# Kernel optimization log

Hardware: AMD Instinct MI355X
Metric: run time of the kernel (lower is better)

Reference implementation:

```python
import jax, jax.numpy as jnp
import numpy as np

EPS = 1e-5  # torch LayerNorm default


def setup_inputs() -> dict:
    key = jax.random.key(0)
    ks = jax.random.split(key, 7)
    B, s, i, c, h = 1, 1024, 512, 8, 8
    scale = 0.1
    return {
        "m": jax.random.normal(ks[0], (B, s, i, c), dtype=jnp.float32),
        "ln_gamma": jnp.ones((c,), dtype=jnp.float32),
        "ln_beta": jnp.zeros((c,), dtype=jnp.float32),
        "Wq": jax.random.normal(ks[1], (c * h, c), dtype=jnp.float32) * scale,
        "Wk": jax.random.normal(ks[2], (c, c), dtype=jnp.float32) * scale,
        "Wv": jax.random.normal(ks[3], (c, c), dtype=jnp.float32) * scale,
        "Wg": jax.random.normal(ks[4], (c * h, c), dtype=jnp.float32) * scale,
        "Wo": jax.random.normal(ks[5], (c, c * h), dtype=jnp.float32) * scale,
        "bo": jnp.zeros((c,), dtype=jnp.float32),
    }


def reference(m, ln_gamma, ln_beta, Wq, Wk, Wv, Wg, Wo, bo):
    c = Wk.shape[0]
    h = Wq.shape[0] // c
    B, s, i, _ = m.shape

    # LayerNorm over the channel dim c
    mu = jnp.mean(m, axis=-1, keepdims=True)
    var = jnp.mean(jnp.square(m - mu), axis=-1, keepdims=True)
    x = (m - mu) * jax.lax.rsqrt(var + EPS) * ln_gamma + ln_beta  # (B,s,i,c)

    # projections (torch Linear: y = x @ W.T)
    q = (x @ Wq.T).reshape(B, s, i, h, c).mean(axis=1)            # (B,i,h,c) mean-pooled query
    k = x @ Wk.T                                                   # (B,s,i,c)
    v = x @ Wv.T                                                   # (B,s,i,c)
    gate = jax.nn.sigmoid(x @ Wg.T).reshape(B, s, i, h, c)        # (B,s,i,h,c)

    # attention logits over the column axis t (=s), softmax along t (dim=-3 of b t i h)
    a = jnp.einsum('bihc,btic->btih', q, k) * (c ** -0.5)          # (B,s,i,h)
    a = jax.nn.softmax(a, axis=1)

    o = gate * jnp.einsum('btih,btic->btihc', a, v)               # (B,s,i,h,c)
    o = o.reshape(B, s, i, h * c)
    return o @ Wo.T + bo                                           # (B,s,i,c)
```

## Files before the change

kernel.cpp:

```cpp
#include <hip/hip_runtime.h>

namespace {
constexpr int S = 1024, I = 512, C = 8, H = 8;
constexpr float LNEPS = 1e-5f;
constexpr float SCALE = 0.35355339059327373f;
}

__device__ __forceinline__ float dot8(const float x[8], float4 a, float4 b) {
    float r = x[0] * a.x;
    r += x[1] * a.y; r += x[2] * a.z; r += x[3] * a.w;
    r += x[4] * b.x; r += x[5] * b.y; r += x[6] * b.z; r += x[7] * b.w;
    return r;
}

__device__ __forceinline__ void ln8(float4 a, float4 b, const float gm[8],
                                    const float bt[8], float x[8]) {
    x[0] = a.x; x[1] = a.y; x[2] = a.z; x[3] = a.w;
    x[4] = b.x; x[5] = b.y; x[6] = b.z; x[7] = b.w;
    float mu = 0.f;
#pragma unroll
    for (int c = 0; c < 8; c++) mu += x[c];
    mu *= 0.125f;
    float var = 0.f;
#pragma unroll
    for (int c = 0; c < 8; c++) { float d = x[c] - mu; var += d * d; }
    var *= 0.125f;
    float inv = rsqrtf(var + LNEPS);
#pragma unroll
    for (int c = 0; c < 8; c++) x[c] = (x[c] - mu) * inv * gm[c] + bt[c];
}

__global__ __launch_bounds__(256) void k1_part(const float* __restrict__ m,
                                               const float* __restrict__ gamma,
                                               const float* __restrict__ beta,
                                               float* __restrict__ part1, int CH1) {
    int g = blockIdx.x * 256 + threadIdx.x;
    int i = g & (I - 1);
    int sc = g >> 9;
    int niter = S / CH1;
    float gm[8], bt[8];
#pragma unroll
    for (int c = 0; c < 8; c++) { gm[c] = gamma[c]; bt[c] = beta[c]; }
    float acc[8];
#pragma unroll
    for (int c = 0; c < 8; c++) acc[c] = 0.f;
    const float4* m4 = (const float4*)m;
    for (int j = 0; j < niter; j++) {
        int row = (sc * niter + j) * I + i;
        float x[8];
        ln8(m4[row * 2], m4[row * 2 + 1], gm, bt, x);
#pragma unroll
        for (int c = 0; c < 8; c++) acc[c] += x[c];
    }
    float4* p4 = (float4*)&part1[((size_t)sc * I + i) * 8];
    p4[0] = make_float4(acc[0], acc[1], acc[2], acc[3]);
    p4[1] = make_float4(acc[4], acc[5], acc[6], acc[7]);
}

__global__ __launch_bounds__(64) void k1b_qk(const float* __restrict__ part1,
                                             const float* __restrict__ Wq,
                                             const float* __restrict__ Wk,
                                             float* __restrict__ qk, int CH1) {
    int i = blockIdx.x, t = threadIdx.x;
    float xs[8];
#pragma unroll
    for (int c = 0; c < 8; c++) xs[c] = 0.f;
    const float4* p4 = (const float4*)part1;
    for (int p = t; p < CH1; p += 64) {
        float4 a = p4[((size_t)p * I + i) * 2], b = p4[((size_t)p * I + i) * 2 + 1];
        xs[0] += a.x; xs[1] += a.y; xs[2] += a.z; xs[3] += a.w;
        xs[4] += b.x; xs[5] += b.y; xs[6] += b.z; xs[7] += b.w;
    }
#pragma unroll
    for (int d = 1; d < 64; d <<= 1)
#pragma unroll
        for (int c = 0; c < 8; c++) xs[c] += __shfl_xor(xs[c], d, 64);
    int h = t >> 3, c2 = t & 7;
    float acc = 0.f;
#pragma unroll
    for (int c = 0; c < 8; c++) {
        float qc = 0.f;
#pragma unroll
        for (int c3 = 0; c3 < 8; c3++) qc += xs[c3] * Wq[(h * 8 + c) * 8 + c3];
        acc += qc * Wk[c * 8 + c2];
    }
    qk[i * 64 + t] = acc * (SCALE / 1024.0f);
}

__global__ __launch_bounds__(256) void k2_part(const float* __restrict__ m,
                                               const float* __restrict__ gamma,
                                               const float* __restrict__ beta,
                                               const float* __restrict__ qk,
                                               float* __restrict__ part2, int CH2) {
    int g = blockIdx.x * 256 + threadIdx.x;
    int i = g & (I - 1);
    int sc = g >> 9;
    int niter = S / CH2;
    float gm[8], bt[8];
#pragma unroll
    for (int c = 0; c < 8; c++) { gm[c] = gamma[c]; bt[c] = beta[c]; }
    const float4* qk4 = (const float4*)qk;
    float4 qv[16];
#pragma unroll
    for (int j = 0; j < 16; j++) qv[j] = qk4[i * 16 + j];
    float acc[8];
#pragma unroll
    for (int h = 0; h < 8; h++) acc[h] = 0.f;
    const float4* m4 = (const float4*)m;
    for (int j0 = 0; j0 < niter; j0 += 4) {
        float x[4][8];
#pragma unroll
        for (int r = 0; r < 4; r++) {
            int row = (sc * niter + j0 + r) * I + i;
            ln8(m4[row * 2], m4[row * 2 + 1], gm, bt, x[r]);
        }
#pragma unroll
        for (int h = 0; h < 8; h++)
#pragma unroll
            for (int r = 0; r < 4; r++)
                acc[h] += __expf(dot8(x[r], qv[h * 2], qv[h * 2 + 1]));
    }
    float4* p4 = (float4*)&part2[((size_t)sc * I + i) * 8];
    p4[0] = make_float4(acc[0], acc[1], acc[2], acc[3]);
    p4[1] = make_float4(acc[4], acc[5], acc[6], acc[7]);
}

__global__ __launch_bounds__(64) void k2b_rden(const float* __restrict__ part2,
                                               float* __restrict__ rden, int CH2) {
    int i = blockIdx.x, t = threadIdx.x;
    float d[8];
#pragma unroll
    for (int c = 0; c < 8; c++) d[c] = 0.f;
    const float4* p4 = (const float4*)part2;
    for (int p = t; p < CH2; p += 64) {
        float4 a = p4[((size_t)p * I + i) * 2], b = p4[((size_t)p * I + i) * 2 + 1];
        d[0] += a.x; d[1] += a.y; d[2] += a.z; d[3] += a.w;
        d[4] += b.x; d[5] += b.y; d[6] += b.z; d[7] += b.w;
    }
#pragma unroll
    for (int dd = 1; dd < 64; dd <<= 1)
#pragma unroll
        for (int c = 0; c < 8; c++) d[c] += __shfl_xor(d[c], dd, 64);
    if (t < 8) rden[i * 8 + t] = 1.0f / d[t];
}

__global__ __launch_bounds__(256) void k3_out(const float* __restrict__ m,
                                              const float* __restrict__ gamma,
                                              const float* __restrict__ beta,
                                              const float* __restrict__ Wv,
                                              const float* __restrict__ Wg,
                                              const float* __restrict__ Wo,
                                              const float* __restrict__ bo,
                                              const float* __restrict__ qk,
                                              const float* __restrict__ rden,
                                              float* __restrict__ out) {
    __shared__ __align__(16) float sWv[64];
    __shared__ __align__(16) float sWg[512];
    __shared__ __align__(16) float sWoT[512];
    int t = threadIdx.x;
    if (t < 64) sWv[t] = Wv[t];
    sWg[t] = Wg[t];
    sWg[t + 256] = Wg[t + 256];
    {
        int j = t & 63, c2 = t >> 6;
        sWoT[j * 8 + c2] = Wo[c2 * 64 + j];
        sWoT[j * 8 + c2 + 4] = Wo[(c2 + 4) * 64 + j];
    }
    __syncthreads();

    float gm[8], bt[8], bov[8];
#pragma unroll
    for (int c = 0; c < 8; c++) { gm[c] = gamma[c]; bt[c] = beta[c]; bov[c] = bo[c]; }

    int g = blockIdx.x * 256 + t;
    int i = g & (I - 1);
    int sg = g >> 9;
    const float4* m4 = (const float4*)m;
    float4* out4 = (float4*)out;

    float4 xa[4], xb[4];
#pragma unroll
    for (int r = 0; r < 4; r++) {
        int row = (sg + 256 * r) * I + i;
        xa[r] = m4[row * 2]; xb[r] = m4[row * 2 + 1];
    }
    float x[4][8];
#pragma unroll
    for (int r = 0; r < 4; r++) ln8(xa[r], xb[r], gm, bt, x[r]);

    const float4* sWv4 = (const float4*)sWv;
    const float4* sWg4 = (const float4*)sWg;
    const float4* sWoT4 = (const float4*)sWoT;

    float v[4][8];
#pragma unroll
    for (int c = 0; c < 8; c++) {
        float4 w0 = sWv4[c * 2], w1 = sWv4[c * 2 + 1];
#pragma unroll
        for (int r = 0; r < 4; r++) v[r][c] = dot8(x[r], w0, w1);
    }

    float oacc[4][8];
#pragma unroll
    for (int r = 0; r < 4; r++)
#pragma unroll
        for (int c2 = 0; c2 < 8; c2++) oacc[r][c2] = bov[c2];

    const float4* qk4 = (const float4*)qk;
#pragma unroll 1
    for (int h = 0; h < 8; h++) {
        float4 q0 = qk4[i * 16 + h * 2], q1 = qk4[i * 16 + h * 2 + 1];
        float rd = rden[i * 8 + h];
        float a_[4];
#pragma unroll
        for (int r = 0; r < 4; r++) a_[r] = __expf(dot8(x[r], q0, q1)) * rd;
#pragma unroll
        for (int c = 0; c < 8; c++) {
            int hc = h * 8 + c;
            float4 wg0 = sWg4[hc * 2], wg1 = sWg4[hc * 2 + 1];
            float o_[4];
#pragma unroll
            for (int r = 0; r < 4; r++) {
                float z = dot8(x[r], wg0, wg1);
                float gate = __builtin_amdgcn_rcpf(1.0f + __expf(-z));
                o_[r] = gate * a_[r] * v[r][c];
            }
            float4 wo0 = sWoT4[hc * 2], wo1 = sWoT4[hc * 2 + 1];
#pragma unroll
            for (int r = 0; r < 4; r++) {
                oacc[r][0] += o_[r] * wo0.x; oacc[r][1] += o_[r] * wo0.y;
                oacc[r][2] += o_[r] * wo0.z; oacc[r][3] += o_[r] * wo0.w;
                oacc[r][4] += o_[r] * wo1.x; oacc[r][5] += o_[r] * wo1.y;
                oacc[r][6] += o_[r] * wo1.z; oacc[r][7] += o_[r] * wo1.w;
            }
        }
    }
#pragma unroll
    for (int r = 0; r < 4; r++) {
        int row = (sg + 256 * r) * I + i;
        out4[row * 2] = make_float4(oacc[r][0], oacc[r][1], oacc[r][2], oacc[r][3]);
        out4[row * 2 + 1] = make_float4(oacc[r][4], oacc[r][5], oacc[r][6], oacc[r][7]);
    }
}

extern "C" void kernel_launch(void* const* d_in, const int* in_sizes, int n_in,
                              void* d_out, int out_size, void* d_ws, size_t ws_size,
                              hipStream_t stream) {
    const float* m     = (const float*)d_in[0];
    const float* gamma = (const float*)d_in[1];
    const float* beta  = (const float*)d_in[2];
    const float* Wq    = (const float*)d_in[3];
    const float* Wk    = (const float*)d_in[4];
    const float* Wv    = (const float*)d_in[5];
    const float* Wg    = (const float*)d_in[6];
    const float* Wo    = (const float*)d_in[7];
    const float* bo    = (const float*)d_in[8];
    float* out = (float*)d_out;

    const size_t small = (size_t)I * 64 * 4 + (size_t)I * 8 * 4;
    int CH1 = 256, CH2 = 256;
    auto need = [&](int c1, int c2) {
        return ((size_t)(c1 + c2) * I * C * 4) + small;
    };
    if (need(256, 256) > ws_size) { CH1 = CH2 = 64; }
    if (need(CH1, CH2) > ws_size) { CH1 = CH2 = 16; }

    float* ws    = (float*)d_ws;
    float* part1 = ws;
    float* part2 = part1 + (size_t)CH1 * I * C;
    float* qk    = part2 + (size_t)CH2 * I * C;
    float* rden  = qk + (size_t)I * 64;

    k1_part<<<I * CH1 / 256, 256, 0, stream>>>(m, gamma, beta, part1, CH1);
    k1b_qk<<<I, 64, 0, stream>>>(part1, Wq, Wk, qk, CH1);
    k2_part<<<I * CH2 / 256, 256, 0, stream>>>(m, gamma, beta, qk, part2, CH2);
    k2b_rden<<<I, 64, 0, stream>>>(part2, rden, CH2);
    k3_out<<<I * 256 / 256, 256, 0, stream>>>(m, gamma, beta, Wv, Wg, Wo, bo, qk,
                                              rden, out);
}
```

Before: 131.7 us.

## Increase parallel split across s, widen reductions, and halve rows per thread in output kernel

The s-axis is now split into 512 chunks instead of 256, so the partial-sum and softmax-denominator kernels each process 2 rows per thread. The reduction kernels use 256 threads with a shared-memory cross-wave combine, and one workspace buffer is shared between both stages. The output kernel runs twice as many blocks, each thread handling 2 rows instead of 4, with launch bounds requesting higher occupancy. The aim is more parallelism and latency hiding, at the cost of more launches' worth of partial traffic and dropping the workspace-size fallback.

```diff
diff --git a/kernel.cpp b/kernel.cpp
--- a/kernel.cpp
+++ b/kernel.cpp
@@ -2,6 +2,7 @@
 
 namespace {
 constexpr int S = 1024, I = 512, C = 8, H = 8;
+constexpr int CH1 = 512, CH2 = 512;
 constexpr float LNEPS = 1e-5f;
 constexpr float SCALE = 0.35355339059327373f;
 }
@@ -33,11 +34,10 @@
 __global__ __launch_bounds__(256) void k1_part(const float* __restrict__ m,
                                                const float* __restrict__ gamma,
                                                const float* __restrict__ beta,
-                                               float* __restrict__ part1, int CH1) {
+                                               float* __restrict__ part1) {
     int g = blockIdx.x * 256 + threadIdx.x;
     int i = g & (I - 1);
     int sc = g >> 9;
-    int niter = S / CH1;
     float gm[8], bt[8];
 #pragma unroll
     for (int c = 0; c < 8; c++) { gm[c] = gamma[c]; bt[c] = beta[c]; }
@@ -45,8 +45,9 @@
 #pragma unroll
     for (int c = 0; c < 8; c++) acc[c] = 0.f;
     const float4* m4 = (const float4*)m;
-    for (int j = 0; j < niter; j++) {
-        int row = (sc * niter + j) * I + i;
+#pragma unroll
+    for (int j = 0; j < S / CH1; j++) {
+        int row = (sc * (S / CH1) + j) * I + i;
         float x[8];
         ln8(m4[row * 2], m4[row * 2 + 1], gm, bt, x);
 #pragma unroll
@@ -57,16 +58,19 @@
     p4[1] = make_float4(acc[4], acc[5], acc[6], acc[7]);
 }
 
-__global__ __launch_bounds__(64) void k1b_qk(const float* __restrict__ part1,
-                                             const float* __restrict__ Wq,
-                                             const float* __restrict__ Wk,
-                                             float* __restrict__ qk, int CH1) {
+__global__ __launch_bounds__(256) void k1b_qk(const float* __restrict__ part1,
+                                              const float* __restrict__ Wq,
+                                              const float* __restrict__ Wk,
+                                              float* __restrict__ qk) {
+    __shared__ float sred[4][8];
     int i = blockIdx.x, t = threadIdx.x;
     float xs[8];
 #pragma unroll
     for (int c = 0; c < 8; c++) xs[c] = 0.f;
     const float4* p4 = (const float4*)part1;
-    for (int p = t; p < CH1; p += 64) {
+#pragma unroll
+    for (int k = 0; k < CH1 / 256; k++) {
+        int p = t + 256 * k;
         float4 a = p4[((size_t)p * I + i) * 2], b = p4[((size_t)p * I + i) * 2 + 1];
         xs[0] += a.x; xs[1] += a.y; xs[2] += a.z; xs[3] += a.w;
         xs[4] += b.x; xs[5] += b.y; xs[6] += b.z; xs[7] += b.w;
@@ -75,64 +79,69 @@
     for (int d = 1; d < 64; d <<= 1)
 #pragma unroll
         for (int c = 0; c < 8; c++) xs[c] += __shfl_xor(xs[c], d, 64);
-    int h = t >> 3, c2 = t & 7;
-    float acc = 0.f;
-#pragma unroll
-    for (int c = 0; c < 8; c++) {
-        float qc = 0.f;
-#pragma unroll
-        for (int c3 = 0; c3 < 8; c3++) qc += xs[c3] * Wq[(h * 8 + c) * 8 + c3];
-        acc += qc * Wk[c * 8 + c2];
-    }
-    qk[i * 64 + t] = acc * (SCALE / 1024.0f);
-}
-
-__global__ __launch_bounds__(256) void k2_part(const float* __restrict__ m,
-                                               const float* __restrict__ gamma,
-                                               const float* __restrict__ beta,
-                                               const float* __restrict__ qk,
-                                               float* __restrict__ part2, int CH2) {
+    if ((t & 63) == 0) {
+#pragma unroll
+        for (int c = 0; c < 8; c++) sred[t >> 6][c] = xs[c];
+    }
+    __syncthreads();
+    if (t < 64) {
+#pragma unroll
+        for (int c = 0; c < 8; c++)
+            xs[c] = sred[0][c] + sred[1][c] + sred[2][c] + sred[3][c];
+        int h = t >> 3, c2 = t & 7;
+        float acc = 0.f;
+#pragma unroll
+        for (int c = 0; c < 8; c++) {
+            float qc = 0.f;
+#pragma unroll
+            for (int c3 = 0; c3 < 8; c3++) qc += xs[c3] * Wq[(h * 8 + c) * 8 + c3];
+            acc += qc * Wk[c * 8 + c2];
+        }
+        qk[i * 64 + t] = acc * (SCALE / 1024.0f);
+    }
+}
+
+__global__ __launch_bounds__(256, 4) void k2_part(const float* __restrict__ m,
+                                                  const float* __restrict__ gamma,
+                                                  const float* __restrict__ beta,
+                                                  const float* __restrict__ qk,
+                                                  float* __restrict__ part2) {
     int g = blockIdx.x * 256 + threadIdx.x;
     int i = g & (I - 1);
     int sc = g >> 9;
-    int niter = S / CH2;
     float gm[8], bt[8];
 #pragma unroll
     for (int c = 0; c < 8; c++) { gm[c] = gamma[c]; bt[c] = beta[c]; }
+    const float4* m4 = (const float4*)m;
+    float x[2][8];
+#pragma unroll
+    for (int r = 0; r < 2; r++) {
+        int row = (sc * 2 + r) * I + i;
+        ln8(m4[row * 2], m4[row * 2 + 1], gm, bt, x[r]);
+    }
     const float4* qk4 = (const float4*)qk;
-    float4 qv[16];
-#pragma unroll
-    for (int j = 0; j < 16; j++) qv[j] = qk4[i * 16 + j];
     float acc[8];
 #pragma unroll
-    for (int h = 0; h < 8; h++) acc[h] = 0.f;
-    const float4* m4 = (const float4*)m;
-    for (int j0 = 0; j0 < niter; j0 += 4) {
-        float x[4][8];
-#pragma unroll
-        for (int r = 0; r < 4; r++) {
-            int row = (sc * niter + j0 + r) * I + i;
-            ln8(m4[row * 2], m4[row * 2 + 1], gm, bt, x[r]);
-        }
-#pragma unroll
-        for (int h = 0; h < 8; h++)
-#pragma unroll
-            for (int r = 0; r < 4; r++)
-                acc[h] += __expf(dot8(x[r], qv[h * 2], qv[h * 2 + 1]));
+    for (int h = 0; h < 8; h++) {
+        float4 q0 = qk4[i * 16 + h * 2], q1 = qk4[i * 16 + h * 2 + 1];
+        acc[h] = __expf(dot8(x[0], q0, q1)) + __expf(dot8(x[1], q0, q1));
     }
     float4* p4 = (float4*)&part2[((size_t)sc * I + i) * 8];
     p4[0] = make_float4(acc[0], acc[1], acc[2], acc[3]);
     p4[1] = make_float4(acc[4], acc[5], acc[6], acc[7]);
 }
 
-__global__ __launch_bounds__(64) void k2b_rden(const float* __restrict__ part2,
-                                               float* __restrict__ rden, int CH2) {
+__global__ __launch_bounds__(256) void k2b_rden(const float* __restrict__ part2,
+                                                float* __restrict__ rden) {
+    __shared__ float sred[4][8];
     int i = blockIdx.x, t = threadIdx.x;
     float d[8];
 #pragma unroll
     for (int c = 0; c < 8; c++) d[c] = 0.f;
     const float4* p4 = (const float4*)part2;
-    for (int p = t; p < CH2; p += 64) {
+#pragma unroll
+    for (int k = 0; k < CH2 / 256; k++) {
+        int p = t + 256 * k;
         float4 a = p4[((size_t)p * I + i) * 2], b = p4[((size_t)p * I + i) * 2 + 1];
         d[0] += a.x; d[1] += a.y; d[2] += a.z; d[3] += a.w;
         d[4] += b.x; d[5] += b.y; d[6] += b.z; d[7] += b.w;
@@ -141,19 +150,26 @@
     for (int dd = 1; dd < 64; dd <<= 1)
 #pragma unroll
         for (int c = 0; c < 8; c++) d[c] += __shfl_xor(d[c], dd, 64);
-    if (t < 8) rden[i * 8 + t] = 1.0f / d[t];
-}
-
-__global__ __launch_bounds__(256) void k3_out(const float* __restrict__ m,
-                                              const float* __restrict__ gamma,
-                                              const float* __restrict__ beta,
-                                              const float* __restrict__ Wv,
-                                              const float* __restrict__ Wg,
-                                              const float* __restrict__ Wo,
-                                              const float* __restrict__ bo,
-                                              const float* __restrict__ qk,
-                                              const float* __restrict__ rden,
-                                              float* __restrict__ out) {
+    if ((t & 63) == 0) {
+#pragma unroll
+        for (int c = 0; c < 8; c++) sred[t >> 6][c] = d[c];
+    }
+    __syncthreads();
+    if (t < 8)
+        rden[i * 8 + t] =
+            1.0f / (sred[0][t] + sred[1][t] + sred[2][t] + sred[3][t]);
+}
+
+__global__ __launch_bounds__(256, 4) void k3_out(const float* __restrict__ m,
+                                                 const float* __restrict__ gamma,
+                                                 const float* __restrict__ beta,
+                                                 const float* __restrict__ Wv,
+                                                 const float* __restrict__ Wg,
+                                                 const float* __restrict__ Wo,
+                                                 const float* __restrict__ bo,
+                                                 const float* __restrict__ qk,
+                                                 const float* __restrict__ rden,
+                                                 float* __restrict__ out) {
     __shared__ __align__(16) float sWv[64];
     __shared__ __align__(16) float sWg[512];
     __shared__ __align__(16) float sWoT[512];
@@ -168,9 +184,9 @@
     }
     __syncthreads();
 
-    float gm[8], bt[8], bov[8];
-#pragma unroll
-    for (int c = 0; c < 8; c++) { gm[c] = gamma[c]; bt[c] = beta[c]; bov[c] = bo[c]; }
+    float gm[8], bt[8];
+#pragma unroll
+    for (int c = 0; c < 8; c++) { gm[c] = gamma[c]; bt[c] = beta[c]; }
 
     int g = blockIdx.x * 256 + t;
     int i = g & (I - 1);
@@ -178,56 +194,53 @@
     const float4* m4 = (const float4*)m;
     float4* out4 = (float4*)out;
 
-    float4 xa[4], xb[4];
-#pragma unroll
-    for (int r = 0; r < 4; r++) {
-        int row = (sg + 256 * r) * I + i;
-        xa[r] = m4[row * 2]; xb[r] = m4[row * 2 + 1];
-    }
-    float x[4][8];
-#pragma unroll
-    for (int r = 0; r < 4; r++) ln8(xa[r], xb[r], gm, bt, x[r]);
+    float x[2][8];
+#pragma unroll
+    for (int r = 0; r < 2; r++) {
+        int row = (sg + 512 * r) * I + i;
+        ln8(m4[row * 2], m4[row * 2 + 1], gm, bt, x[r]);
+    }
 
     const float4* sWv4 = (const float4*)sWv;
     const float4* sWg4 = (const float4*)sWg;
     const float4* sWoT4 = (const float4*)sWoT;
 
-    float v[4][8];
+    float v[2][8];
 #pragma unroll
     for (int c = 0; c < 8; c++) {
         float4 w0 = sWv4[c * 2], w1 = sWv4[c * 2 + 1];
 #pragma unroll
-        for (int r = 0; r < 4; r++) v[r][c] = dot8(x[r], w0, w1);
-    }
-
-    float oacc[4][8];
-#pragma unroll
-    for (int r = 0; r < 4; r++)
-#pragma unroll
-        for (int c2 = 0; c2 < 8; c2++) oacc[r][c2] = bov[c2];
+        for (int r = 0; r < 2; r++) v[r][c] = dot8(x[r], w0, w1);
+    }
+
+    float oacc[2][8];
+#pragma unroll
+    for (int r = 0; r < 2; r++)
+#pragma unroll
+        for (int c2 = 0; c2 < 8; c2++) oacc[r][c2] = bo[c2];
 
     const float4* qk4 = (const float4*)qk;
 #pragma unroll 1
     for (int h = 0; h < 8; h++) {
         float4 q0 = qk4[i * 16 + h * 2], q1 = qk4[i * 16 + h * 2 + 1];
         float rd = rden[i * 8 + h];
-        float a_[4];
-#pragma unroll
-        for (int r = 0; r < 4; r++) a_[r] = __expf(dot8(x[r], q0, q1)) * rd;
+        float a_[2];
+#pragma unroll
+        for (int r = 0; r < 2; r++) a_[r] = __expf(dot8(x[r], q0, q1)) * rd;
 #pragma unroll
         for (int c = 0; c < 8; c++) {
             int hc = h * 8 + c;
             float4 wg0 = sWg4[hc * 2], wg1 = sWg4[hc * 2 + 1];
-            float o_[4];
-#pragma unroll
-            for (int r = 0; r < 4; r++) {
+            float o_[2];
+#pragma unroll
+            for (int r = 0; r < 2; r++) {
                 float z = dot8(x[r], wg0, wg1);
                 float gate = __builtin_amdgcn_rcpf(1.0f + __expf(-z));
                 o_[r] = gate * a_[r] * v[r][c];
             }
             float4 wo0 = sWoT4[hc * 2], wo1 = sWoT4[hc * 2 + 1];
 #pragma unroll
-            for (int r = 0; r < 4; r++) {
+            for (int r = 0; r < 2; r++) {
                 oacc[r][0] += o_[r] * wo0.x; oacc[r][1] += o_[r] * wo0.y;
                 oacc[r][2] += o_[r] * wo0.z; oacc[r][3] += o_[r] * wo0.w;
                 oacc[r][4] += o_[r] * wo1.x; oacc[r][5] += o_[r] * wo1.y;
@@ -236,8 +249,8 @@
         }
     }
 #pragma unroll
-    for (int r = 0; r < 4; r++) {
-        int row = (sg + 256 * r) * I + i;
+    for (int r = 0; r < 2; r++) {
+        int row = (sg + 512 * r) * I + i;
         out4[row * 2] = make_float4(oacc[r][0], oacc[r][1], oacc[r][2], oacc[r][3]);
         out4[row * 2 + 1] = make_float4(oacc[r][4], oacc[r][5], oacc[r][6], oacc[r][7]);
     }
@@ -257,24 +270,15 @@
     const float* bo    = (const float*)d_in[8];
     float* out = (float*)d_out;
 
-    const size_t small = (size_t)I * 64 * 4 + (size_t)I * 8 * 4;
-    int CH1 = 256, CH2 = 256;
-    auto need = [&](int c1, int c2) {
-        return ((size_t)(c1 + c2) * I * C * 4) + small;
-    };
-    if (need(256, 256) > ws_size) { CH1 = CH2 = 64; }
-    if (need(CH1, CH2) > ws_size) { CH1 = CH2 = 16; }
-
-    float* ws    = (float*)d_ws;
-    float* part1 = ws;
-    float* part2 = part1 + (size_t)CH1 * I * C;
-    float* qk    = part2 + (size_t)CH2 * I * C;
-    float* rden  = qk + (size_t)I * 64;
-
-    k1_part<<<I * CH1 / 256, 256, 0, stream>>>(m, gamma, beta, part1, CH1);
-    k1b_qk<<<I, 64, 0, stream>>>(part1, Wq, Wk, qk, CH1);
-    k2_part<<<I * CH2 / 256, 256, 0, stream>>>(m, gamma, beta, qk, part2, CH2);
-    k2b_rden<<<I, 64, 0, stream>>>(part2, rden, CH2);
-    k3_out<<<I * 256 / 256, 256, 0, stream>>>(m, gamma, beta, Wv, Wg, Wo, bo, qk,
+    float* ws   = (float*)d_ws;
+    float* part = ws;
+    float* qk   = part + (size_t)CH1 * I * C;
+    float* rden = qk + (size_t)I * 64;
+
+    k1_part<<<I * CH1 / 256, 256, 0, stream>>>(m, gamma, beta, part);
+    k1b_qk<<<I, 256, 0, stream>>>(part, Wq, Wk, qk);
+    k2_part<<<I * CH2 / 256, 256, 0, stream>>>(m, gamma, beta, qk, part);
+    k2b_rden<<<I, 256, 0, stream>>>(part, rden);
+    k3_out<<<I * 512 / 256, 256, 0, stream>>>(m, gamma, beta, Wv, Wg, Wo, bo, qk,
                                               rden, out);
 }
```

Result: slower. 140.5 us (+6.7%).
